# Kernel tuning notes

Measured on AMD Instinct MI355X. Metric: run time of the kernel, lower is better.

## Reference

```python
import jax, jax.numpy as jnp
import numpy as np

B, T, N, F, H, R, E = 32, 8, 150, 16, 32, 4, 16


def _gconv(X, Af, Wf):
    # t-product graph conv (Kilmer t-product = circular conv over relation axis,
    # implemented facewise in the Fourier domain): ifft( fft(adj) @ fft(X) @ fft(W) )
    Xf = jnp.fft.fft(X, axis=-1)                      # [b,n,f,r] complex
    Y = jnp.einsum('nmr,bmfr->bnfr', Af, Xf)          # aggregate over nodes
    Y = jnp.einsum('bnfr,for->bnor', Y, Wf)           # feature transform
    return jnp.fft.ifft(Y, axis=-1).real


def _cell(X, Hs, Af, Wf, Bb):
    # TensorGRUCell. NOTE: faithful to the source, H_tilda reuses conv_hr
    # (conv_hh is defined but never used in the original forward).
    Wxz, Wxr, Wxh, Whz, Whr = Wf
    bz, br, bh = Bb[0], Bb[1], Bb[2]                  # [H,R], broadcasts over [b,n,H,R]
    Z = jax.nn.sigmoid(_gconv(X, Af, Wxz) + _gconv(Hs, Af, Whz) + bz)
    Rg = jax.nn.sigmoid(_gconv(X, Af, Wxr) + _gconv(Hs, Af, Whr) + br)
    Ht = jnp.tanh(_gconv(X, Af, Wxh) + _gconv(Rg * Hs, Af, Whr) + bh)
    return Z * Hs + (1.0 - Z) * Ht


def setup_inputs() -> dict:
    key = jax.random.key(0)
    ks = jax.random.split(key, 16)
    kai = lambda k, shp, fan: (jax.random.normal(k, shp, jnp.float32)
                               * np.float32(np.sqrt(2.0 / fan)))
    d = {}
    d['inputs'] = jax.random.normal(ks[0], (B, T, N, F, R), jnp.float32)
    d['U'] = kai(ks[1], (N, E, R), N)
    # layer 0 (input_dim=F)
    d['Wxz0'] = kai(ks[2], (F, H, R), F)
    d['Wxr0'] = kai(ks[3], (F, H, R), F)
    d['Wxh0'] = kai(ks[4], (F, H, R), F)
    d['Whz0'] = kai(ks[5], (H, H, R), H)
    d['Whr0'] = kai(ks[6], (H, H, R), H)
    d['B0'] = kai(ks[7], (3, H, R), 3)
    # layer 1 (input_dim=H)
    d['Wxz1'] = kai(ks[8], (H, H, R), H)
    d['Wxr1'] = kai(ks[9], (H, H, R), H)
    d['Wxh1'] = kai(ks[10], (H, H, R), H)
    d['Whz1'] = kai(ks[11], (H, H, R), H)
    d['Whr1'] = kai(ks[12], (H, H, R), H)
    d['B1'] = kai(ks[13], (3, H, R), 3)
    return d


def reference(inputs, U, Wxz0, Wxr0, Wxh0, Whz0, Whr0, B0,
              Wxz1, Wxr1, Wxh1, Whz1, Whr1, B1):
    # adaptive adjacency: softmax(relu(tprod(U, U^T)), dim=1)
    Uf = jnp.fft.fft(U, axis=-1)                      # [N,E,R] complex
    A = jnp.fft.ifft(jnp.einsum('ner,mer->nmr', Uf, Uf), axis=-1).real
    adj = jax.nn.softmax(jax.nn.relu(A), axis=1)      # [N,N,R]

    Af = jnp.fft.fft(adj, axis=-1)
    Wf0 = tuple(jnp.fft.fft(w, axis=-1) for w in (Wxz0, Wxr0, Wxh0, Whz0, Whr0))
    Wf1 = tuple(jnp.fft.fft(w, axis=-1) for w in (Wxz1, Wxr1, Wxh1, Whz1, Whr1))

    b, t, n, f, r = inputs.shape
    h = Whz0.shape[0]
    z0 = jnp.zeros((b, n, h, r), inputs.dtype)

    # t = 0: layer1 consumes the *current* layer0 output
    o0 = _cell(inputs[:, 0], z0, Af, Wf0, B0)
    o1 = _cell(o0, z0, Af, Wf1, B1)

    # t > 0: faithful to source, layer1 consumes the *previous timestep's*
    # layer0 output (temp_out[t-1][i-1]) with hidden temp_out[t-1][i].
    def step(carry, Xt):
        p0, p1 = carry
        n0 = _cell(Xt, p0, Af, Wf0, B0)
        n1 = _cell(p0, p1, Af, Wf1, B1)
        return (n0, n1), n1

    Xs = jnp.moveaxis(inputs[:, 1:], 1, 0)            # [T-1,B,N,F,R]
    (c0, c1), ys = jax.lax.scan(step, (o0, o1), Xs)

    out = jnp.concatenate([o1[None], ys], axis=0)     # [T,B,N,H,R]
    out = jnp.moveaxis(out, 0, 1)                     # [B,T,N,H,R]
    h_last = jnp.stack([c0, c1])                      # [L,B,N,H,R]
    return out, h_last
```

## Files before the change

kernel.cpp:

```cpp
#include <hip/hip_runtime.h>
#include <math.h>

#define NN 150
#define BB 32
#define TT 8
#define FF 16
#define HH 32
#define ROWS (NN*BB)
#define NCIN (BB*FF)
#define NCH  (BB*HH)
#define ADJ_LD 160
#define KPAD 68

#define SZ_ADJF (4*NN*ADJ_LD)
#define SZ_WA0  (4*48*32*4)
#define SZ_WA1  (4*64*32*4)
#define SZ_WB   (32*32*4)
#define SZ_STATE (ROWS*HH*4)
#define SZ_PIN  (4*NN*NCIN)

__device__ __forceinline__ float sigmoidf_(float x){ return 1.f/(1.f+expf(-x)); }

__device__ __forceinline__ float comp_of4(float x0, float x1, float x2, float x3, int c) {
  return c==0 ? (x0+x1+x2+x3) : c==1 ? (x0-x2) : c==2 ? (x3-x1) : (x0-x1+x2-x3);
}


__global__ __launch_bounds__(256) void k_adj(const float* __restrict__ U, float* __restrict__ adjF) {
  __shared__ float Ufl[NN*16*4];
  __shared__ float Arow[NN*4];
  __shared__ float red[256];
  __shared__ float mxs[4], isms[4];
  int n = blockIdx.x, tid = threadIdx.x;
  for (int idx = tid; idx < NN*16; idx += 256) {
    const float* s = U + (size_t)idx*4;
    float x0=s[0], x1=s[1], x2=s[2], x3=s[3];
    Ufl[idx*4+0] = x0+x1+x2+x3;
    Ufl[idx*4+1] = x0-x2;
    Ufl[idx*4+2] = x3-x1;
    Ufl[idx*4+3] = x0-x1+x2-x3;
  }
  __syncthreads();
  if (tid < NN) {
    int m = tid;
    float a0=0, ar=0, ai=0, a2=0;
    #pragma unroll
    for (int e = 0; e < 16; ++e) {
      const float* un = &Ufl[(n*16+e)*4];
      const float* um = &Ufl[(m*16+e)*4];
      a0 += un[0]*um[0];
      ar += un[1]*um[1] - un[2]*um[2];
      ai += un[1]*um[2] + un[2]*um[1];
      a2 += un[3]*um[3];
    }
    float r0 = 0.25f*(a0 + 2.f*ar + a2);
    float r1 = 0.25f*(a0 - 2.f*ai - a2);
    float r2 = 0.25f*(a0 - 2.f*ar + a2);
    float r3 = 0.25f*(a0 + 2.f*ai - a2);
    Arow[m*4+0] = fmaxf(r0, 0.f);
    Arow[m*4+1] = fmaxf(r1, 0.f);
    Arow[m*4+2] = fmaxf(r2, 0.f);
    Arow[m*4+3] = fmaxf(r3, 0.f);
  }
  __syncthreads();
  for (int r = 0; r < 4; ++r) {
    float v = (tid < NN) ? Arow[tid*4+r] : -1e30f;
    red[tid] = v; __syncthreads();
    for (int s = 128; s > 0; s >>= 1) { if (tid < s) red[tid] = fmaxf(red[tid], red[tid+s]); __syncthreads(); }
    if (tid == 0) mxs[r] = red[0];
    __syncthreads();
    float e = (tid < NN) ? expf(Arow[tid*4+r] - mxs[r]) : 0.f;
    red[tid] = e; __syncthreads();
    for (int s = 128; s > 0; s >>= 1) { if (tid < s) red[tid] += red[tid+s]; __syncthreads(); }
    if (tid == 0) isms[r] = 1.f / red[0];
    __syncthreads();
    if (tid < NN) Arow[tid*4+r] = e * isms[r];
    __syncthreads();
  }
  if (tid < NN) {
    int m = tid;
    float e0=Arow[m*4+0], e1=Arow[m*4+1], e2=Arow[m*4+2], e3=Arow[m*4+3];
    size_t base = (size_t)n*ADJ_LD + m;
    size_t cs = (size_t)NN*ADJ_LD;
    adjF[base]      = e0+e1+e2+e3;
    adjF[base+cs]   = e0-e2;
    adjF[base+2*cs] = e3-e1;
    adjF[base+3*cs] = e0-e1+e2-e3;
  } else if (tid < ADJ_LD) {
    size_t base = (size_t)n*ADJ_LD + tid;
    size_t cs = (size_t)NN*ADJ_LD;
    adjF[base] = 0.f; adjF[base+cs] = 0.f; adjF[base+2*cs] = 0.f; adjF[base+3*cs] = 0.f;
  }
}

__global__ __launch_bounds__(256) void k_wts(
    const float* __restrict__ Wxz0, const float* __restrict__ Wxr0, const float* __restrict__ Wxh0,
    const float* __restrict__ Whz0, const float* __restrict__ Whr0,
    const float* __restrict__ Wxz1, const float* __restrict__ Wxr1, const float* __restrict__ Wxh1,
    const float* __restrict__ Whz1, const float* __restrict__ Whr1,
    float* __restrict__ WA0p, float* __restrict__ WA1p,
    float* __restrict__ WB0p, float* __restrict__ WB1p) {
  int idx = blockIdx.x*256 + threadIdx.x;
  const float* src = nullptr;
  float* dst; int didx; int c;
  if (idx < SZ_WA0) {
    c = idx / 6144;
    int rem = idx % 6144;
    int k = rem >> 7, og = (rem >> 2) & 31, q = rem & 3;
    if (q == 0) src = (k < FF) ? Wxz0 + ((size_t)k*HH + og)*4 : Whz0 + ((size_t)(k-FF)*HH + og)*4;
    else if (q == 1) src = (k < FF) ? Wxr0 + ((size_t)k*HH + og)*4 : Whr0 + ((size_t)(k-FF)*HH + og)*4;
    else if (q == 2 && k < FF) src = Wxh0 + ((size_t)k*HH + og)*4;
    dst = WA0p; didx = idx;
  } else if (idx < SZ_WA0 + SZ_WA1) {
    int id = idx - SZ_WA0;
    c = id >> 13;
    int rem = id & 8191;
    int k = rem >> 7, og = (rem >> 2) & 31, q = rem & 3;
    if (q == 0) src = (k < HH) ? Wxz1 + ((size_t)k*HH + og)*4 : Whz1 + ((size_t)(k-HH)*HH + og)*4;
    else if (q == 1) src = (k < HH) ? Wxr1 + ((size_t)k*HH + og)*4 : Whr1 + ((size_t)(k-HH)*HH + og)*4;
    else if (q == 2 && k < HH) src = Wxh1 + ((size_t)k*HH + og)*4;
    dst = WA1p; didx = id;
  } else if (idx < SZ_WA0 + SZ_WA1 + SZ_WB) {
    int id = idx - (SZ_WA0 + SZ_WA1);
    int k = id >> 7, o = (id >> 2) & 31;
    c = id & 3;
    src = Whr0 + ((size_t)k*HH + o)*4;
    dst = WB0p; didx = id;
  } else if (idx < SZ_WA0 + SZ_WA1 + 2*SZ_WB) {
    int id = idx - (SZ_WA0 + SZ_WA1 + SZ_WB);
    int k = id >> 7, o = (id >> 2) & 31;
    c = id & 3;
    src = Whr1 + ((size_t)k*HH + o)*4;
    dst = WB1p; didx = id;
  } else return;
  float v0=0,v1=0,v2=0,v3=0;
  if (src) { v0=src[0]; v1=src[1]; v2=src[2]; v3=src[3]; }
  dst[didx] = comp_of4(v0,v1,v2,v3,c);
}

struct AggParams {
  const float* X0; const float* X1; const float* X2;
  float* P0; float* P1; float* P2;
  int ncol0, ncol1, ncol2;
  int base1, base2, njobs, rawt, nb;
};
__global__ __launch_bounds__(256,4) void k_agg(AggParams pr, const float* __restrict__ adjF,
                                               const float* __restrict__ inp) {
  __shared__ float As[4*32*37];
  __shared__ float Xs[4*32*36];
  int bid = blockIdx.x;
  int part = (bid >= pr.nb) ? 1 : 0;
  if (part) bid -= pr.nb;
  const float* X; float* P; int ncol; int tile; bool raw = false;
  if (pr.njobs >= 3 && bid >= pr.base2) { X = pr.X2; P = pr.P2; ncol = pr.ncol2; tile = bid - pr.base2; }
  else if (pr.njobs >= 2 && bid >= pr.base1) { X = pr.X1; P = pr.P1; ncol = pr.ncol1; tile = bid - pr.base1; }
  else { X = pr.X0; P = pr.P0; ncol = pr.ncol0; tile = bid; raw = (pr.rawt >= 0); }
  P += (size_t)part * 4 * NN * ncol;
  int kbeg = part ? 96 : 0;
  int kend = part ? NN : 96;
  int n0 = (tile % 5) * 32;
  int col0 = (tile / 5) * 32;
  int tid = threadIdx.x;
  int ti = tid & 31, tj = tid >> 5;
  int j0 = tj * 4;
  float a0[4]={}, aR[4]={}, aI[4]={}, a2v[4]={};

  float4 pa[4];
  float4 px[4];

  #define LOAD_A(K0)                                                         \
    _Pragma("unroll")                                                        \
    for (int u = 0; u < 4; ++u) {                                            \
      int e = tid + u*256;                                                   \
      int c = e >> 8, rem = e & 255, i = rem >> 3, kq = rem & 7;             \
      int nn_ = n0 + i;                                                      \
      pa[u] = make_float4(0,0,0,0);                                          \
      if (nn_ < NN) pa[u] = *(const float4*)(adjF + ((size_t)c*NN + nn_)*ADJ_LD + (K0) + kq*4); \
    }
  #define STORE_A()                                                          \
    _Pragma("unroll")                                                        \
    for (int u = 0; u < 4; ++u) {                                            \
      int e = tid + u*256;                                                   \
      int c = e >> 8, rem = e & 255, i = rem >> 3, kq = rem & 7;             \
      As[(c*32 + kq*4+0)*37 + i] = pa[u].x;                                  \
      As[(c*32 + kq*4+1)*37 + i] = pa[u].y;                                  \
      As[(c*32 + kq*4+2)*37 + i] = pa[u].z;                                  \
      As[(c*32 + kq*4+3)*37 + i] = pa[u].w;                                  \
    }
  #define LOAD_X(K0)                                                         \
    if (raw) {                                                               \
      int q = tid & 7, kk = tid >> 3;                                        \
      int mm = (K0) + kk;                                                    \
      int col = col0 + q*4;                                                  \
      int b = col >> 4, f = col & 15;                                        \
      px[0]=px[1]=px[2]=px[3]=make_float4(0,0,0,0);                          \
      if (mm < NN) {                                                         \
        const float* s = inp + (((size_t)(b*TT + pr.rawt)*NN + mm)*FF + f)*4;\
        px[0] = *(const float4*)(s+0);                                       \
        px[1] = *(const float4*)(s+4);                                       \
        px[2] = *(const float4*)(s+8);                                       \
        px[3] = *(const float4*)(s+12);                                      \
      }                                                                      \
    } else {                                                                 \
      _Pragma("unroll")                                                      \
      for (int u = 0; u < 4; ++u) {                                          \
        int e = tid + u*256;                                                 \
        int c = e >> 8, rem = e & 255, kk = rem >> 3, q = rem & 7;           \
        int mm = (K0) + kk;                                                  \
        px[u] = make_float4(0,0,0,0);                                        \
        if (mm < NN) px[u] = *(const float4*)(X + ((size_t)c*NN + mm)*ncol + col0 + q*4); \
      }                                                                      \
    }
  #define STORE_X()                                                          \
    if (raw) {                                                               \
      int q = tid & 7, kk = tid >> 3;                                        \
      float4 r0 = px[0], r1 = px[1], r2 = px[2], r3 = px[3];                 \
      float4 w;                                                              \
      w = make_float4(r0.x+r0.y+r0.z+r0.w, r1.x+r1.y+r1.z+r1.w, r2.x+r2.y+r2.z+r2.w, r3.x+r3.y+r3.z+r3.w); \
      *(float4*)&Xs[(0*32+kk)*36 + q*4] = w;                                 \
      w = make_float4(r0.x-r0.z, r1.x-r1.z, r2.x-r2.z, r3.x-r3.z);           \
      *(float4*)&Xs[(1*32+kk)*36 + q*4] = w;                                 \
      w = make_float4(r0.w-r0.y, r1.w-r1.y, r2.w-r2.y, r3.w-r3.y);           \
      *(float4*)&Xs[(2*32+kk)*36 + q*4] = w;                                 \
      w = make_float4(r0.x-r0.y+r0.z-r0.w, r1.x-r1.y+r1.z-r1.w, r2.x-r2.y+r2.z-r2.w, r3.x-r3.y+r3.z-r3.w); \
      *(float4*)&Xs[(3*32+kk)*36 + q*4] = w;                                 \
    } else {                                                                 \
      _Pragma("unroll")                                                      \
      for (int u = 0; u < 4; ++u) {                                          \
        int e = tid + u*256;                                                 \
        int c = e >> 8, rem = e & 255, kk = rem >> 3, q = rem & 7;           \
        *(float4*)&Xs[(c*32+kk)*36 + q*4] = px[u];                           \
      }                                                                      \
    }

  LOAD_A(kbeg)
  LOAD_X(kbeg)
  for (int k0 = kbeg; k0 < kend; k0 += 32) {
    STORE_A()
    STORE_X()
    __syncthreads();
    int k0n = k0 + 32;
    if (k0n < kend) {
      LOAD_A(k0n)
      LOAD_X(k0n)
    }
    #pragma unroll 4
    for (int k = 0; k < 32; ++k) {
      float A0 = As[(0*32+k)*37 + ti];
      float A1 = As[(1*32+k)*37 + ti];
      float A2 = As[(2*32+k)*37 + ti];
      float A3 = As[(3*32+k)*37 + ti];
      float4 x0 = *(float4*)&Xs[(0*32+k)*36 + j0];
      float4 x1 = *(float4*)&Xs[(1*32+k)*36 + j0];
      float4 x2 = *(float4*)&Xs[(2*32+k)*36 + j0];
      float4 x3 = *(float4*)&Xs[(3*32+k)*36 + j0];
      float X0v[4]={x0.x,x0.y,x0.z,x0.w}, X1v[4]={x1.x,x1.y,x1.z,x1.w};
      float X2v[4]={x2.x,x2.y,x2.z,x2.w}, X3v[4]={x3.x,x3.y,x3.z,x3.w};
      #pragma unroll
      for (int j = 0; j < 4; ++j) {
        a0[j] += A0*X0v[j];
        aR[j] += A1*X1v[j] - A2*X2v[j];
        aI[j] += A1*X2v[j] + A2*X1v[j];
        a2v[j] += A3*X3v[j];
      }
    }
    __syncthreads();
  }
  int nn_ = n0 + ti;
  if (nn_ < NN) {
    size_t cs = (size_t)NN*ncol;
    size_t rb = (size_t)nn_*ncol + col0 + j0;
    *(float4*)&P[rb]      = make_float4(a0[0],a0[1],a0[2],a0[3]);
    *(float4*)&P[rb+cs]   = make_float4(aR[0],aR[1],aR[2],aR[3]);
    *(float4*)&P[rb+2*cs] = make_float4(aI[0],aI[1],aI[2],aI[3]);
    *(float4*)&P[rb+3*cs] = make_float4(a2v[0],a2v[1],a2v[2],a2v[3]);
  }
}

struct FAJob {
  const float* Px;
  const float* Ph;
  const float* W;
  const float* bias;
  const float* hprev;
  float* Z; float* T1; float* Mf;
  int zh;
};
struct FAParams { FAJob j[2]; };

template<int KTOT, int KX>
__device__ __forceinline__ void fusedA_body(const FAJob& jb, float* Ps, float* Ws) {
  const int row0 = blockIdx.x * 16;
  const int tid = threadIdx.x;
  const int og = tid & 31;
  const int rg = tid >> 5;
  const int r0 = rg*2, r1 = rg*2 + 1;
  const size_t psx = (size_t)4*ROWS*KX;
  const size_t psh = (size_t)4*ROWS*HH;
  constexpr int K4 = KTOT/4;
  for (int e = tid; e < 16*4*K4; e += 256) {
    int k4 = e % K4; int c = (e / K4) & 3; int r = e / (K4*4);
    int k = k4*4;
    int row = row0 + r;
    float4 v;
    if (k < KX) {
      const float* a = &jb.Px[((size_t)c*ROWS + row)*KX + k];
      float4 va = *(const float4*)a;
      float4 vb = *(const float4*)(a + psx);
      v = make_float4(va.x+vb.x, va.y+vb.y, va.z+vb.z, va.w+vb.w);
    } else if (jb.zh) {
      v = make_float4(0,0,0,0);
    } else {
      const float* a = &jb.Ph[((size_t)c*ROWS + row)*HH + (k - KX)];
      float4 va = *(const float4*)a;
      float4 vb = *(const float4*)(a + psh);
      v = make_float4(va.x+vb.x, va.y+vb.y, va.z+vb.z, va.w+vb.w);
    }
    *(float4*)&Ps[(r*4 + c)*KPAD + k] = v;
  }
  float acc0[2][3]={{0,0,0},{0,0,0}}, accR[2][3]={{0,0,0},{0,0,0}};
  float accI[2][3]={{0,0,0},{0,0,0}}, acc2[2][3]={{0,0,0},{0,0,0}};
  constexpr int NCHK = KTOT/16;
  const float4* Wg = (const float4*)jb.W;
  for (int cc = 0; cc < NCHK; ++cc) {
    __syncthreads();
    #pragma unroll
    for (int u = 0; u < 8; ++u) {
      int f = tid + u*256;
      int c = f >> 9, rem = f & 511;
      float4 v = Wg[((size_t)c*KTOT + cc*16)*32 + rem];
      *(float4*)&Ws[((size_t)c*512 + rem)*4] = v;
    }
    __syncthreads();
    #pragma unroll 4
    for (int kk = 0; kk < 16; ++kk) {
      int k = cc*16 + kk;
      float p0a = Ps[(r0*4+0)*KPAD + k];
      float p1a = Ps[(r0*4+1)*KPAD + k];
      float p2a = Ps[(r0*4+2)*KPAD + k];
      float p3a = Ps[(r0*4+3)*KPAD + k];
      float p0b = Ps[(r1*4+0)*KPAD + k];
      float p1b = Ps[(r1*4+1)*KPAD + k];
      float p2b = Ps[(r1*4+2)*KPAD + k];
      float p3b = Ps[(r1*4+3)*KPAD + k];
      float4 w0 = *(float4*)&Ws[((0*16+kk)*32+og)*4];
      float4 w1 = *(float4*)&Ws[((1*16+kk)*32+og)*4];
      float4 w2 = *(float4*)&Ws[((2*16+kk)*32+og)*4];
      float4 w3 = *(float4*)&Ws[((3*16+kk)*32+og)*4];
      float W0v[3]={w0.x,w0.y,w0.z}, W1v[3]={w1.x,w1.y,w1.z};
      float W2v[3]={w2.x,w2.y,w2.z}, W3v[3]={w3.x,w3.y,w3.z};
      #pragma unroll
      for (int q = 0; q < 3; ++q) {
        acc0[0][q] += p0a*W0v[q];
        acc0[1][q] += p0b*W0v[q];
        accR[0][q] += p1a*W1v[q] - p2a*W2v[q];
        accR[1][q] += p1b*W1v[q] - p2b*W2v[q];
        accI[0][q] += p1a*W2v[q] + p2a*W1v[q];
        accI[1][q] += p1b*W2v[q] + p2b*W1v[q];
        acc2[0][q] += p3a*W3v[q];
        acc2[1][q] += p3b*W3v[q];
      }
    }
  }
  const float* bz = jb.bias + (0*HH + og)*4;
  const float* br = jb.bias + (1*HH + og)*4;
  const float* bh = jb.bias + (2*HH + og)*4;
  float bzv[4] = {bz[0],bz[1],bz[2],bz[3]};
  float brv[4] = {br[0],br[1],br[2],br[3]};
  float bhv[4] = {bh[0],bh[1],bh[2],bh[3]};
  #pragma unroll
  for (int rr = 0; rr < 2; ++rr) {
    int row = row0 + rg*2 + rr;
    float ys[3][4];
    #pragma unroll
    for (int q = 0; q < 3; ++q) {
      float Y0 = acc0[rr][q], Yr = accR[rr][q], Yi = accI[rr][q], Y2 = acc2[rr][q];
      ys[q][0] = 0.25f*(Y0 + 2.f*Yr + Y2);
      ys[q][1] = 0.25f*(Y0 - 2.f*Yi - Y2);
      ys[q][2] = 0.25f*(Y0 - 2.f*Yr + Y2);
      ys[q][3] = 0.25f*(Y0 + 2.f*Yi - Y2);
    }
    float4 z = make_float4(sigmoidf_(ys[0][0]+bzv[0]), sigmoidf_(ys[0][1]+bzv[1]),
                           sigmoidf_(ys[0][2]+bzv[2]), sigmoidf_(ys[0][3]+bzv[3]));
    *(float4*)&jb.Z[((size_t)row*HH + og)*4] = z;
    float4 hp = make_float4(0,0,0,0);
    if (!jb.zh) hp = *(const float4*)&jb.hprev[((size_t)row*HH + og)*4];
    float m0 = sigmoidf_(ys[1][0]+brv[0]) * hp.x;
    float m1 = sigmoidf_(ys[1][1]+brv[1]) * hp.y;
    float m2 = sigmoidf_(ys[1][2]+brv[2]) * hp.z;
    float m3 = sigmoidf_(ys[1][3]+brv[3]) * hp.w;
    size_t mb = (size_t)row*HH + og;
    size_t cs = (size_t)ROWS*HH;
    jb.Mf[mb]      = m0+m1+m2+m3;
    jb.Mf[mb+cs]   = m0-m2;
    jb.Mf[mb+2*cs] = m3-m1;
    jb.Mf[mb+3*cs] = m0-m1+m2-m3;
    float4 tv = make_float4(ys[2][0]+bhv[0], ys[2][1]+bhv[1], ys[2][2]+bhv[2], ys[2][3]+bhv[3]);
    *(float4*)&jb.T1[((size_t)row*HH + og)*4] = tv;
  }
}

__global__ __launch_bounds__(256,3) void k_fusedA_both(FAParams pr) {
  __shared__ float Ps[16*4*KPAD];
  __shared__ float Ws[8192];
  if (blockIdx.y == 0) fusedA_body<48,16>(pr.j[0], Ps, Ws);
  else                 fusedA_body<64,32>(pr.j[1], Ps, Ws);
}
__global__ __launch_bounds__(256,3) void k_fusedA_L0(FAParams pr) {
  __shared__ float Ps[16*4*KPAD];
  __shared__ float Ws[8192];
  fusedA_body<48,16>(pr.j[0], Ps, Ws);
}
__global__ __launch_bounds__(256,3) void k_fusedA_L1(FAParams pr) {
  __shared__ float Ps[16*4*KPAD];
  __shared__ float Ws[8192];
  fusedA_body<64,32>(pr.j[1], Ps, Ws);
}

struct FBJob {
  const float* Pm; const float* W; const float* T1; const float* Z;
  float* h; float* hf; float* outp; float* hlast;
  int t, zh, wout;
};
struct FBParams { FBJob j[2]; };
__global__ __launch_bounds__(256,4) void k_fusedB(FBParams pr) {
  __shared__ float Ps[16*32*4];
  __shared__ float Ws[32*32*4];
  FBJob jb = pr.j[blockIdx.y];
  int row0 = blockIdx.x * 16;
  int tid = threadIdx.x;
  int rg = tid >> 5, o = tid & 31;
  int r0 = rg*2, r1 = r0 + 1;
  float acc0[2]={0,0}, accR[2]={0,0}, accI[2]={0,0}, acc2[2]={0,0};
  if (!jb.zh) {
    #pragma unroll
    for (int u = 0; u < 4; ++u) {
      int f = tid + u*256;
      ((float4*)Ws)[f] = ((const float4*)jb.W)[f];
    }
    const size_t psh = (size_t)4*ROWS*HH;
    #pragma unroll
    for (int u = 0; u < 2; ++u) {
      int e = tid + u*256;
      int r = e >> 5, k = e & 31;
      int row = row0 + r;
      float4 v;
      float* vv = (float*)&v;
      #pragma unroll
      for (int c = 0; c < 4; ++c) {
        size_t ix = ((size_t)c*ROWS + row)*HH + k;
        vv[c] = jb.Pm[ix] + jb.Pm[ix + psh];
      }
      *(float4*)&Ps[(r*32 + k)*4] = v;
    }
    __syncthreads();
    #pragma unroll 8
    for (int k = 0; k < 32; ++k) {
      float4 pA = *(const float4*)&Ps[(r0*32 + k)*4];
      float4 pB = *(const float4*)&Ps[(r1*32 + k)*4];
      float4 w  = *(const float4*)&Ws[(k*32 + o)*4];
      acc0[0] += pA.x*w.x;  acc0[1] += pB.x*w.x;
      accR[0] += pA.y*w.y - pA.z*w.z;  accR[1] += pB.y*w.y - pB.z*w.z;
      accI[0] += pA.y*w.z + pA.z*w.y;  accI[1] += pB.y*w.z + pB.z*w.y;
      acc2[0] += pA.w*w.w;  acc2[1] += pB.w*w.w;
    }
  }
  #pragma unroll
  for (int rr = 0; rr < 2; ++rr) {
    int row = row0 + rg*2 + rr;
    float y0 = 0.25f*(acc0[rr] + 2.f*accR[rr] + acc2[rr]);
    float y1 = 0.25f*(acc0[rr] - 2.f*accI[rr] - acc2[rr]);
    float y2 = 0.25f*(acc0[rr] - 2.f*accR[rr] + acc2[rr]);
    float y3 = 0.25f*(acc0[rr] + 2.f*accI[rr] - acc2[rr]);
    float4 t1 = *(const float4*)&jb.T1[((size_t)row*HH + o)*4];
    float h0v = tanhf(t1.x + y0);
    float h1v = tanhf(t1.y + y1);
    float h2v = tanhf(t1.z + y2);
    float h3v = tanhf(t1.w + y3);
    float4 z = *(const float4*)&jb.Z[((size_t)row*HH + o)*4];
    float4 hp = make_float4(0,0,0,0);
    if (!jb.zh) hp = *(const float4*)&jb.h[((size_t)row*HH + o)*4];
    float n0v = z.x*hp.x + (1.f-z.x)*h0v;
    float n1v = z.y*hp.y + (1.f-z.y)*h1v;
    float n2v = z.z*hp.z + (1.f-z.z)*h2v;
    float n3v = z.w*hp.w + (1.f-z.w)*h3v;
    *(float4*)&jb.h[((size_t)row*HH + o)*4] = make_float4(n0v,n1v,n2v,n3v);
    size_t hb = (size_t)row*HH + o, cs = (size_t)ROWS*HH;
    jb.hf[hb]      = n0v+n1v+n2v+n3v;
    jb.hf[hb+cs]   = n0v-n2v;
    jb.hf[hb+2*cs] = n3v-n1v;
    jb.hf[hb+3*cs] = n0v-n1v+n2v-n3v;
    int n = row >> 5, b = row & 31;
    if (jb.wout) {
      float* dst = jb.outp + (((size_t)b*TT + jb.t)*NN + n)*(HH*4) + o*4;
      *(float4*)dst = make_float4(n0v,n1v,n2v,n3v);
    }
    if (jb.hlast) {
      float* dst = jb.hlast + ((size_t)(b*NN + n))*(HH*4) + o*4;
      *(float4*)dst = make_float4(n0v,n1v,n2v,n3v);
    }
  }
}

extern "C" void kernel_launch(void* const* d_in, const int* in_sizes, int n_in,
                              void* d_out, int out_size, void* d_ws, size_t ws_size,
                              hipStream_t stream) {
  const float* inp  = (const float*)d_in[0];
  const float* U    = (const float*)d_in[1];
  const float* Wxz0 = (const float*)d_in[2];
  const float* Wxr0 = (const float*)d_in[3];
  const float* Wxh0 = (const float*)d_in[4];
  const float* Whz0 = (const float*)d_in[5];
  const float* Whr0 = (const float*)d_in[6];
  const float* B0   = (const float*)d_in[7];
  const float* Wxz1 = (const float*)d_in[8];
  const float* Wxr1 = (const float*)d_in[9];
  const float* Wxh1 = (const float*)d_in[10];
  const float* Whz1 = (const float*)d_in[11];
  const float* Whr1 = (const float*)d_in[12];
  const float* B1   = (const float*)d_in[13];
  float* out = (float*)d_out;

  float* ws = (float*)d_ws;
  float* ADJF = ws;  ws += SZ_ADJF;
  float* WA0  = ws;  ws += SZ_WA0;
  float* WA1  = ws;  ws += SZ_WA1;
  float* WB0  = ws;  ws += SZ_WB;
  float* WB1  = ws;  ws += SZ_WB;
  float* H0   = ws;  ws += SZ_STATE;
  float* H1   = ws;  ws += SZ_STATE;
  float* H0F  = ws;  ws += SZ_STATE;
  float* H1F  = ws;  ws += SZ_STATE;
  float* PIN  = ws;  ws += 2*SZ_PIN;
  float* PH0  = ws;  ws += 2*SZ_STATE;
  float* PH1  = ws;  ws += 2*SZ_STATE;
  float* PM0  = ws;  ws += 2*SZ_STATE;
  float* PM1  = ws;  ws += 2*SZ_STATE;
  float* M0F  = ws;  ws += SZ_STATE;
  float* M1F  = ws;  ws += SZ_STATE;
  float* Z0   = ws;  ws += SZ_STATE;
  float* Z1   = ws;  ws += SZ_STATE;
  float* T10  = ws;  ws += SZ_STATE;
  float* T11  = ws;  ws += SZ_STATE;

  k_adj<<<NN, 256, 0, stream>>>(U, ADJF);
  k_wts<<<(SZ_WA0+SZ_WA1+2*SZ_WB+255)/256, 256, 0, stream>>>(
      Wxz0,Wxr0,Wxh0,Whz0,Whr0,Wxz1,Wxr1,Wxh1,Whz1,Whr1,WA0,WA1,WB0,WB1);

  {
    AggParams p; p.X0=nullptr; p.P0=PIN; p.ncol0=NCIN;
    p.X1=nullptr; p.P1=nullptr; p.ncol1=0; p.X2=nullptr; p.P2=nullptr; p.ncol2=0;
    p.base1=0; p.base2=0; p.njobs=1; p.rawt=0; p.nb=80;
    k_agg<<<160, 256, 0, stream>>>(p, ADJF, inp);
  }
  {
    FAParams p;
    p.j[0] = FAJob{PIN, nullptr, WA0, B0, nullptr, Z0, T10, M0F, 1};
    p.j[1] = p.j[0];
    k_fusedA_L0<<<dim3(300,1), 256, 0, stream>>>(p);
  }
  {
    FBParams p;
    p.j[0] = FBJob{nullptr, WB0, T10, Z0, H0, H0F, nullptr, nullptr, 0, 1, 0};
    p.j[1] = p.j[0];
    k_fusedB<<<dim3(300,1), 256, 0, stream>>>(p);
  }
  {
    AggParams p; p.X0=H0F; p.P0=PH0; p.ncol0=NCH;
    p.X1=nullptr; p.P1=nullptr; p.ncol1=0; p.X2=nullptr; p.P2=nullptr; p.ncol2=0;
    p.base1=0; p.base2=0; p.njobs=1; p.rawt=-1; p.nb=160;
    k_agg<<<320, 256, 0, stream>>>(p, ADJF, inp);
  }
  {
    FAParams p;
    p.j[0] = FAJob{PH0, nullptr, WA1, B1, nullptr, Z1, T11, M1F, 1};
    p.j[1] = p.j[0];
    k_fusedA_L1<<<dim3(300,1), 256, 0, stream>>>(p);
  }
  {
    FBParams p;
    p.j[0] = FBJob{nullptr, WB1, T11, Z1, H1, H1F, out, nullptr, 0, 1, 1};
    p.j[1] = p.j[0];
    k_fusedB<<<dim3(300,1), 256, 0, stream>>>(p);
  }

  float* hlast0 = out + (size_t)BB*TT*NN*HH*4;
  float* hlast1 = hlast0 + (size_t)BB*NN*HH*4;
  for (int t = 1; t < TT; ++t) {
    {
      AggParams p;
      p.X0=nullptr; p.P0=PIN; p.ncol0=NCIN;
      p.X1=H0F; p.P1=PH0; p.ncol1=NCH;
      p.X2=H1F; p.P2=PH1; p.ncol2=NCH;
      p.base1=80; p.base2=240; p.njobs=3; p.rawt=t; p.nb=400;
      k_agg<<<800, 256, 0, stream>>>(p, ADJF, inp);
    }
    {
      FAParams p;
      p.j[0] = FAJob{PIN, PH0, WA0, B0, H0, Z0, T10, M0F, 0};
      p.j[1] = FAJob{PH0, PH1, WA1, B1, H1, Z1, T11, M1F, 0};
      k_fusedA_both<<<dim3(300,2), 256, 0, stream>>>(p);
    }
    {
      AggParams p;
      p.X0=M0F; p.P0=PM0; p.ncol0=NCH;
      p.X1=M1F; p.P1=PM1; p.ncol1=NCH;
      p.X2=nullptr; p.P2=nullptr; p.ncol2=0;
      p.base1=160; p.base2=0; p.njobs=2; p.rawt=-1; p.nb=320;
      k_agg<<<640, 256, 0, stream>>>(p, ADJF, inp);
    }
    {
      int last = (t == TT-1);
      FBParams p;
      p.j[0] = FBJob{PM0, WB0, T10, Z0, H0, H0F, nullptr, last ? hlast0 : nullptr, t, 0, 0};
      p.j[1] = FBJob{PM1, WB1, T11, Z1, H1, H1F, out,     last ? hlast1 : nullptr, t, 0, 1};
      k_fusedB<<<dim3(300,2), 256, 0, stream>>>(p);
    }
  }
}
```

Baseline: 846.2 us.

## Hoist input aggregation for all timesteps out of recurrence and interleave shared-memory layouts

Precomputes the adjacency aggregation of the raw inputs for every timestep in one up-front launch, removing that work from each recurrent step's aggregation kernel. Merges the adjacency and weight-prep kernels into one launch. Also changes the shared-memory layouts of the aggregation A tile and the fusedA P tile so the four Fourier components are interleaved, allowing single float4 reads. The cost is a larger workspace holding all timesteps' aggregated inputs.

```diff
diff --git a/kernel.cpp b/kernel.cpp
--- a/kernel.cpp
+++ b/kernel.cpp
@@ -10,7 +10,7 @@
 #define NCIN (BB*FF)
 #define NCH  (BB*HH)
 #define ADJ_LD 160
-#define KPAD 68
+#define PS_LD 65
 
 #define SZ_ADJF (4*NN*ADJ_LD)
 #define SZ_WA0  (4*48*32*4)
@@ -26,81 +26,83 @@
 }
 
 
-__global__ __launch_bounds__(256) void k_adj(const float* __restrict__ U, float* __restrict__ adjF) {
-  __shared__ float Ufl[NN*16*4];
-  __shared__ float Arow[NN*4];
-  __shared__ float red[256];
-  __shared__ float mxs[4], isms[4];
-  int n = blockIdx.x, tid = threadIdx.x;
-  for (int idx = tid; idx < NN*16; idx += 256) {
-    const float* s = U + (size_t)idx*4;
-    float x0=s[0], x1=s[1], x2=s[2], x3=s[3];
-    Ufl[idx*4+0] = x0+x1+x2+x3;
-    Ufl[idx*4+1] = x0-x2;
-    Ufl[idx*4+2] = x3-x1;
-    Ufl[idx*4+3] = x0-x1+x2-x3;
-  }
-  __syncthreads();
-  if (tid < NN) {
-    int m = tid;
-    float a0=0, ar=0, ai=0, a2=0;
-    #pragma unroll
-    for (int e = 0; e < 16; ++e) {
-      const float* un = &Ufl[(n*16+e)*4];
-      const float* um = &Ufl[(m*16+e)*4];
-      a0 += un[0]*um[0];
-      ar += un[1]*um[1] - un[2]*um[2];
-      ai += un[1]*um[2] + un[2]*um[1];
-      a2 += un[3]*um[3];
-    }
-    float r0 = 0.25f*(a0 + 2.f*ar + a2);
-    float r1 = 0.25f*(a0 - 2.f*ai - a2);
-    float r2 = 0.25f*(a0 - 2.f*ar + a2);
-    float r3 = 0.25f*(a0 + 2.f*ai - a2);
-    Arow[m*4+0] = fmaxf(r0, 0.f);
-    Arow[m*4+1] = fmaxf(r1, 0.f);
-    Arow[m*4+2] = fmaxf(r2, 0.f);
-    Arow[m*4+3] = fmaxf(r3, 0.f);
-  }
-  __syncthreads();
-  for (int r = 0; r < 4; ++r) {
-    float v = (tid < NN) ? Arow[tid*4+r] : -1e30f;
-    red[tid] = v; __syncthreads();
-    for (int s = 128; s > 0; s >>= 1) { if (tid < s) red[tid] = fmaxf(red[tid], red[tid+s]); __syncthreads(); }
-    if (tid == 0) mxs[r] = red[0];
-    __syncthreads();
-    float e = (tid < NN) ? expf(Arow[tid*4+r] - mxs[r]) : 0.f;
-    red[tid] = e; __syncthreads();
-    for (int s = 128; s > 0; s >>= 1) { if (tid < s) red[tid] += red[tid+s]; __syncthreads(); }
-    if (tid == 0) isms[r] = 1.f / red[0];
-    __syncthreads();
-    if (tid < NN) Arow[tid*4+r] = e * isms[r];
-    __syncthreads();
-  }
-  if (tid < NN) {
-    int m = tid;
-    float e0=Arow[m*4+0], e1=Arow[m*4+1], e2=Arow[m*4+2], e3=Arow[m*4+3];
-    size_t base = (size_t)n*ADJ_LD + m;
-    size_t cs = (size_t)NN*ADJ_LD;
-    adjF[base]      = e0+e1+e2+e3;
-    adjF[base+cs]   = e0-e2;
-    adjF[base+2*cs] = e3-e1;
-    adjF[base+3*cs] = e0-e1+e2-e3;
-  } else if (tid < ADJ_LD) {
-    size_t base = (size_t)n*ADJ_LD + tid;
-    size_t cs = (size_t)NN*ADJ_LD;
-    adjF[base] = 0.f; adjF[base+cs] = 0.f; adjF[base+2*cs] = 0.f; adjF[base+3*cs] = 0.f;
-  }
-}
-
-__global__ __launch_bounds__(256) void k_wts(
+__global__ __launch_bounds__(256) void k_pre(
+    const float* __restrict__ U, float* __restrict__ adjF,
     const float* __restrict__ Wxz0, const float* __restrict__ Wxr0, const float* __restrict__ Wxh0,
     const float* __restrict__ Whz0, const float* __restrict__ Whr0,
     const float* __restrict__ Wxz1, const float* __restrict__ Wxr1, const float* __restrict__ Wxh1,
     const float* __restrict__ Whz1, const float* __restrict__ Whr1,
     float* __restrict__ WA0p, float* __restrict__ WA1p,
     float* __restrict__ WB0p, float* __restrict__ WB1p) {
-  int idx = blockIdx.x*256 + threadIdx.x;
+  __shared__ float Ufl[NN*16*4];
+  __shared__ float Arow[NN*4];
+  __shared__ float red[256];
+  __shared__ float mxs[4], isms[4];
+  int tid = threadIdx.x;
+  if (blockIdx.x < NN) {
+    int n = blockIdx.x;
+    for (int idx = tid; idx < NN*16; idx += 256) {
+      const float* s = U + (size_t)idx*4;
+      float x0=s[0], x1=s[1], x2=s[2], x3=s[3];
+      Ufl[idx*4+0] = x0+x1+x2+x3;
+      Ufl[idx*4+1] = x0-x2;
+      Ufl[idx*4+2] = x3-x1;
+      Ufl[idx*4+3] = x0-x1+x2-x3;
+    }
+    __syncthreads();
+    if (tid < NN) {
+      int m = tid;
+      float a0=0, ar=0, ai=0, a2=0;
+      #pragma unroll
+      for (int e = 0; e < 16; ++e) {
+        const float* un = &Ufl[(n*16+e)*4];
+        const float* um = &Ufl[(m*16+e)*4];
+        a0 += un[0]*um[0];
+        ar += un[1]*um[1] - un[2]*um[2];
+        ai += un[1]*um[2] + un[2]*um[1];
+        a2 += un[3]*um[3];
+      }
+      float r0 = 0.25f*(a0 + 2.f*ar + a2);
+      float r1 = 0.25f*(a0 - 2.f*ai - a2);
+      float r2 = 0.25f*(a0 - 2.f*ar + a2);
+      float r3 = 0.25f*(a0 + 2.f*ai - a2);
+      Arow[m*4+0] = fmaxf(r0, 0.f);
+      Arow[m*4+1] = fmaxf(r1, 0.f);
+      Arow[m*4+2] = fmaxf(r2, 0.f);
+      Arow[m*4+3] = fmaxf(r3, 0.f);
+    }
+    __syncthreads();
+    for (int r = 0; r < 4; ++r) {
+      float v = (tid < NN) ? Arow[tid*4+r] : -1e30f;
+      red[tid] = v; __syncthreads();
+      for (int s = 128; s > 0; s >>= 1) { if (tid < s) red[tid] = fmaxf(red[tid], red[tid+s]); __syncthreads(); }
+      if (tid == 0) mxs[r] = red[0];
+      __syncthreads();
+      float e = (tid < NN) ? expf(Arow[tid*4+r] - mxs[r]) : 0.f;
+      red[tid] = e; __syncthreads();
+      for (int s = 128; s > 0; s >>= 1) { if (tid < s) red[tid] += red[tid+s]; __syncthreads(); }
+      if (tid == 0) isms[r] = 1.f / red[0];
+      __syncthreads();
+      if (tid < NN) Arow[tid*4+r] = e * isms[r];
+      __syncthreads();
+    }
+    if (tid < NN) {
+      int m = tid;
+      float e0=Arow[m*4+0], e1=Arow[m*4+1], e2=Arow[m*4+2], e3=Arow[m*4+3];
+      size_t base = (size_t)n*ADJ_LD + m;
+      size_t cs = (size_t)NN*ADJ_LD;
+      adjF[base]      = e0+e1+e2+e3;
+      adjF[base+cs]   = e0-e2;
+      adjF[base+2*cs] = e3-e1;
+      adjF[base+3*cs] = e0-e1+e2-e3;
+    } else if (tid < ADJ_LD) {
+      size_t base = (size_t)n*ADJ_LD + tid;
+      size_t cs = (size_t)NN*ADJ_LD;
+      adjF[base] = 0.f; adjF[base+cs] = 0.f; adjF[base+2*cs] = 0.f; adjF[base+3*cs] = 0.f;
+    }
+    return;
+  }
+  int idx = (blockIdx.x - NN)*256 + tid;
   const float* src = nullptr;
   float* dst; int didx; int c;
   if (idx < SZ_WA0) {
@@ -138,35 +140,21 @@
   dst[didx] = comp_of4(v0,v1,v2,v3,c);
 }
 
-struct AggParams {
-  const float* X0; const float* X1; const float* X2;
-  float* P0; float* P1; float* P2;
-  int ncol0, ncol1, ncol2;
-  int base1, base2, njobs, rawt, nb;
-};
-__global__ __launch_bounds__(256,4) void k_agg(AggParams pr, const float* __restrict__ adjF,
-                                               const float* __restrict__ inp) {
-  __shared__ float As[4*32*37];
-  __shared__ float Xs[4*32*36];
-  int bid = blockIdx.x;
-  int part = (bid >= pr.nb) ? 1 : 0;
-  if (part) bid -= pr.nb;
-  const float* X; float* P; int ncol; int tile; bool raw = false;
-  if (pr.njobs >= 3 && bid >= pr.base2) { X = pr.X2; P = pr.P2; ncol = pr.ncol2; tile = bid - pr.base2; }
-  else if (pr.njobs >= 2 && bid >= pr.base1) { X = pr.X1; P = pr.P1; ncol = pr.ncol1; tile = bid - pr.base1; }
-  else { X = pr.X0; P = pr.P0; ncol = pr.ncol0; tile = bid; raw = (pr.rawt >= 0); }
-  P += (size_t)part * 4 * NN * ncol;
+template<bool RAW>
+__device__ __forceinline__ void agg_body(const float* __restrict__ adjF,
+                                         const float* __restrict__ X,
+                                         const float* __restrict__ inp,
+                                         float* __restrict__ P, int ncol,
+                                         int tile, int part, int rawt,
+                                         float* As, float* Xs, int tid) {
   int kbeg = part ? 96 : 0;
   int kend = part ? NN : 96;
   int n0 = (tile % 5) * 32;
   int col0 = (tile / 5) * 32;
-  int tid = threadIdx.x;
   int ti = tid & 31, tj = tid >> 5;
   int j0 = tj * 4;
   float a0[4]={}, aR[4]={}, aI[4]={}, a2v[4]={};
-
-  float4 pa[4];
-  float4 px[4];
+  float4 pa[4], px[4];
 
   #define LOAD_A(K0)                                                         \
     _Pragma("unroll")                                                        \
@@ -182,20 +170,20 @@
     for (int u = 0; u < 4; ++u) {                                            \
       int e = tid + u*256;                                                   \
       int c = e >> 8, rem = e & 255, i = rem >> 3, kq = rem & 7;             \
-      As[(c*32 + kq*4+0)*37 + i] = pa[u].x;                                  \
-      As[(c*32 + kq*4+1)*37 + i] = pa[u].y;                                  \
-      As[(c*32 + kq*4+2)*37 + i] = pa[u].z;                                  \
-      As[(c*32 + kq*4+3)*37 + i] = pa[u].w;                                  \
+      As[((kq*4+0)*33 + i)*4 + c] = pa[u].x;                                 \
+      As[((kq*4+1)*33 + i)*4 + c] = pa[u].y;                                 \
+      As[((kq*4+2)*33 + i)*4 + c] = pa[u].z;                                 \
+      As[((kq*4+3)*33 + i)*4 + c] = pa[u].w;                                 \
     }
   #define LOAD_X(K0)                                                         \
-    if (raw) {                                                               \
+    if (RAW) {                                                               \
       int q = tid & 7, kk = tid >> 3;                                        \
       int mm = (K0) + kk;                                                    \
       int col = col0 + q*4;                                                  \
       int b = col >> 4, f = col & 15;                                        \
       px[0]=px[1]=px[2]=px[3]=make_float4(0,0,0,0);                          \
       if (mm < NN) {                                                         \
-        const float* s = inp + (((size_t)(b*TT + pr.rawt)*NN + mm)*FF + f)*4;\
+        const float* s = inp + (((size_t)(b*TT + rawt)*NN + mm)*FF + f)*4;   \
         px[0] = *(const float4*)(s+0);                                       \
         px[1] = *(const float4*)(s+4);                                       \
         px[2] = *(const float4*)(s+8);                                       \
@@ -212,7 +200,7 @@
       }                                                                      \
     }
   #define STORE_X()                                                          \
-    if (raw) {                                                               \
+    if (RAW) {                                                               \
       int q = tid & 7, kk = tid >> 3;                                        \
       float4 r0 = px[0], r1 = px[1], r2 = px[2], r3 = px[3];                 \
       float4 w;                                                              \
@@ -246,10 +234,7 @@
     }
     #pragma unroll 4
     for (int k = 0; k < 32; ++k) {
-      float A0 = As[(0*32+k)*37 + ti];
-      float A1 = As[(1*32+k)*37 + ti];
-      float A2 = As[(2*32+k)*37 + ti];
-      float A3 = As[(3*32+k)*37 + ti];
+      float4 a4 = *(float4*)&As[(k*33 + ti)*4];
       float4 x0 = *(float4*)&Xs[(0*32+k)*36 + j0];
       float4 x1 = *(float4*)&Xs[(1*32+k)*36 + j0];
       float4 x2 = *(float4*)&Xs[(2*32+k)*36 + j0];
@@ -258,14 +243,18 @@
       float X2v[4]={x2.x,x2.y,x2.z,x2.w}, X3v[4]={x3.x,x3.y,x3.z,x3.w};
       #pragma unroll
       for (int j = 0; j < 4; ++j) {
-        a0[j] += A0*X0v[j];
-        aR[j] += A1*X1v[j] - A2*X2v[j];
-        aI[j] += A1*X2v[j] + A2*X1v[j];
-        a2v[j] += A3*X3v[j];
+        a0[j]  += a4.x*X0v[j];
+        aR[j]  += a4.y*X1v[j] - a4.z*X2v[j];
+        aI[j]  += a4.y*X2v[j] + a4.z*X1v[j];
+        a2v[j] += a4.w*X3v[j];
       }
     }
     __syncthreads();
   }
+  #undef LOAD_A
+  #undef STORE_A
+  #undef LOAD_X
+  #undef STORE_X
   int nn_ = n0 + ti;
   if (nn_ < NN) {
     size_t cs = (size_t)NN*ncol;
@@ -275,6 +264,38 @@
     *(float4*)&P[rb+2*cs] = make_float4(aI[0],aI[1],aI[2],aI[3]);
     *(float4*)&P[rb+3*cs] = make_float4(a2v[0],a2v[1],a2v[2],a2v[3]);
   }
+}
+
+#define AGG_AS 4224
+#define AGG_XS 4608
+
+__global__ __launch_bounds__(256,4) void k_aggIN(const float* __restrict__ adjF,
+                                                 const float* __restrict__ inp,
+                                                 float* __restrict__ PIN) {
+  __shared__ float As[AGG_AS];
+  __shared__ float Xs[AGG_XS];
+  int u = blockIdx.x;
+  int t = u / 160, rem = u % 160, part = rem / 80, tile = rem % 80;
+  float* P = PIN + (size_t)t*2*SZ_PIN + (size_t)part*SZ_PIN;
+  agg_body<true>(adjF, nullptr, inp, P, NCIN, tile, part, t, As, Xs, threadIdx.x);
+}
+
+struct AggParams {
+  const float* X0; const float* X1;
+  float* P0; float* P1;
+  int base1, njobs, nb;
+};
+__global__ __launch_bounds__(256,4) void k_agg(AggParams pr, const float* __restrict__ adjF) {
+  __shared__ float As[AGG_AS];
+  __shared__ float Xs[AGG_XS];
+  int bid = blockIdx.x;
+  int part = (bid >= pr.nb) ? 1 : 0;
+  if (part) bid -= pr.nb;
+  const float* X; float* P; int tile;
+  if (pr.njobs >= 2 && bid >= pr.base1) { X = pr.X1; P = pr.P1; tile = bid - pr.base1; }
+  else { X = pr.X0; P = pr.P0; tile = bid; }
+  P += (size_t)part * SZ_STATE;
+  agg_body<false>(adjF, X, nullptr, P, NCH, tile, part, -1, As, Xs, threadIdx.x);
 }
 
 struct FAJob {
@@ -316,7 +337,10 @@
       float4 vb = *(const float4*)(a + psh);
       v = make_float4(va.x+vb.x, va.y+vb.y, va.z+vb.z, va.w+vb.w);
     }
-    *(float4*)&Ps[(r*4 + c)*KPAD + k] = v;
+    Ps[(r*PS_LD + k+0)*4 + c] = v.x;
+    Ps[(r*PS_LD + k+1)*4 + c] = v.y;
+    Ps[(r*PS_LD + k+2)*4 + c] = v.z;
+    Ps[(r*PS_LD + k+3)*4 + c] = v.w;
   }
   float acc0[2][3]={{0,0,0},{0,0,0}}, accR[2][3]={{0,0,0},{0,0,0}};
   float accI[2][3]={{0,0,0},{0,0,0}}, acc2[2][3]={{0,0,0},{0,0,0}};
@@ -335,14 +359,8 @@
     #pragma unroll 4
     for (int kk = 0; kk < 16; ++kk) {
       int k = cc*16 + kk;
-      float p0a = Ps[(r0*4+0)*KPAD + k];
-      float p1a = Ps[(r0*4+1)*KPAD + k];
-      float p2a = Ps[(r0*4+2)*KPAD + k];
-      float p3a = Ps[(r0*4+3)*KPAD + k];
-      float p0b = Ps[(r1*4+0)*KPAD + k];
-      float p1b = Ps[(r1*4+1)*KPAD + k];
-      float p2b = Ps[(r1*4+2)*KPAD + k];
-      float p3b = Ps[(r1*4+3)*KPAD + k];
+      float4 pA = *(float4*)&Ps[(r0*PS_LD + k)*4];
+      float4 pB = *(float4*)&Ps[(r1*PS_LD + k)*4];
       float4 w0 = *(float4*)&Ws[((0*16+kk)*32+og)*4];
       float4 w1 = *(float4*)&Ws[((1*16+kk)*32+og)*4];
       float4 w2 = *(float4*)&Ws[((2*16+kk)*32+og)*4];
@@ -351,14 +369,14 @@
       float W2v[3]={w2.x,w2.y,w2.z}, W3v[3]={w3.x,w3.y,w3.z};
       #pragma unroll
       for (int q = 0; q < 3; ++q) {
-        acc0[0][q] += p0a*W0v[q];
-        acc0[1][q] += p0b*W0v[q];
-        accR[0][q] += p1a*W1v[q] - p2a*W2v[q];
-        accR[1][q] += p1b*W1v[q] - p2b*W2v[q];
-        accI[0][q] += p1a*W2v[q] + p2a*W1v[q];
-        accI[1][q] += p1b*W2v[q] + p2b*W1v[q];
-        acc2[0][q] += p3a*W3v[q];
-        acc2[1][q] += p3b*W3v[q];
+        acc0[0][q] += pA.x*W0v[q];
+        acc0[1][q] += pB.x*W0v[q];
+        accR[0][q] += pA.y*W1v[q] - pA.z*W2v[q];
+        accR[1][q] += pB.y*W1v[q] - pB.z*W2v[q];
+        accI[0][q] += pA.y*W2v[q] + pA.z*W1v[q];
+        accI[1][q] += pB.y*W2v[q] + pB.z*W1v[q];
+        acc2[0][q] += pA.w*W3v[q];
+        acc2[1][q] += pB.w*W3v[q];
       }
     }
   }
@@ -400,19 +418,21 @@
   }
 }
 
+#define FA_PS (16*PS_LD*4)
+
 __global__ __launch_bounds__(256,3) void k_fusedA_both(FAParams pr) {
-  __shared__ float Ps[16*4*KPAD];
+  __shared__ float Ps[FA_PS];
   __shared__ float Ws[8192];
   if (blockIdx.y == 0) fusedA_body<48,16>(pr.j[0], Ps, Ws);
   else                 fusedA_body<64,32>(pr.j[1], Ps, Ws);
 }
 __global__ __launch_bounds__(256,3) void k_fusedA_L0(FAParams pr) {
-  __shared__ float Ps[16*4*KPAD];
+  __shared__ float Ps[FA_PS];
   __shared__ float Ws[8192];
   fusedA_body<48,16>(pr.j[0], Ps, Ws);
 }
 __global__ __launch_bounds__(256,3) void k_fusedA_L1(FAParams pr) {
-  __shared__ float Ps[16*4*KPAD];
+  __shared__ float Ps[FA_PS];
   __shared__ float Ws[8192];
   fusedA_body<64,32>(pr.j[1], Ps, Ws);
 }
@@ -531,7 +551,7 @@
   float* H1   = ws;  ws += SZ_STATE;
   float* H0F  = ws;  ws += SZ_STATE;
   float* H1F  = ws;  ws += SZ_STATE;
-  float* PIN  = ws;  ws += 2*SZ_PIN;
+  float* PIN  = ws;  ws += (size_t)TT*2*SZ_PIN;
   float* PH0  = ws;  ws += 2*SZ_STATE;
   float* PH1  = ws;  ws += 2*SZ_STATE;
   float* PM0  = ws;  ws += 2*SZ_STATE;
@@ -543,16 +563,14 @@
   float* T10  = ws;  ws += SZ_STATE;
   float* T11  = ws;  ws += SZ_STATE;
 
-  k_adj<<<NN, 256, 0, stream>>>(U, ADJF);
-  k_wts<<<(SZ_WA0+SZ_WA1+2*SZ_WB+255)/256, 256, 0, stream>>>(
-      Wxz0,Wxr0,Wxh0,Whz0,Whr0,Wxz1,Wxr1,Wxh1,Whz1,Whr1,WA0,WA1,WB0,WB1);
-
-  {
-    AggParams p; p.X0=nullptr; p.P0=PIN; p.ncol0=NCIN;
-    p.X1=nullptr; p.P1=nullptr; p.ncol1=0; p.X2=nullptr; p.P2=nullptr; p.ncol2=0;
-    p.base1=0; p.base2=0; p.njobs=1; p.rawt=0; p.nb=80;
-    k_agg<<<160, 256, 0, stream>>>(p, ADJF, inp);
-  }
+  k_pre<<<NN + (SZ_WA0+SZ_WA1+2*SZ_WB+255)/256, 256, 0, stream>>>(
+      U, ADJF, Wxz0,Wxr0,Wxh0,Whz0,Whr0, Wxz1,Wxr1,Wxh1,Whz1,Whr1, WA0,WA1,WB0,WB1);
+
+  k_aggIN<<<TT*2*80, 256, 0, stream>>>(ADJF, inp, PIN);
+
+  float* hlast0 = out + (size_t)BB*TT*NN*HH*4;
+  float* hlast1 = hlast0 + (size_t)BB*NN*HH*4;
+
   {
     FAParams p;
     p.j[0] = FAJob{PIN, nullptr, WA0, B0, nullptr, Z0, T10, M0F, 1};
@@ -566,10 +584,9 @@
     k_fusedB<<<dim3(300,1), 256, 0, stream>>>(p);
   }
   {
-    AggParams p; p.X0=H0F; p.P0=PH0; p.ncol0=NCH;
-    p.X1=nullptr; p.P1=nullptr; p.ncol1=0; p.X2=nullptr; p.P2=nullptr; p.ncol2=0;
-    p.base1=0; p.base2=0; p.njobs=1; p.rawt=-1; p.nb=160;
-    k_agg<<<320, 256, 0, stream>>>(p, ADJF, inp);
+    AggParams p; p.X0=H0F; p.P0=PH0; p.X1=nullptr; p.P1=nullptr;
+    p.base1=0; p.njobs=1; p.nb=160;
+    k_agg<<<320, 256, 0, stream>>>(p, ADJF);
   }
   {
     FAParams p;
@@ -584,30 +601,22 @@
     k_fusedB<<<dim3(300,1), 256, 0, stream>>>(p);
   }
 
-  float* hlast0 = out + (size_t)BB*TT*NN*HH*4;
-  float* hlast1 = hlast0 + (size_t)BB*NN*HH*4;
   for (int t = 1; t < TT; ++t) {
     {
-      AggParams p;
-      p.X0=nullptr; p.P0=PIN; p.ncol0=NCIN;
-      p.X1=H0F; p.P1=PH0; p.ncol1=NCH;
-      p.X2=H1F; p.P2=PH1; p.ncol2=NCH;
-      p.base1=80; p.base2=240; p.njobs=3; p.rawt=t; p.nb=400;
-      k_agg<<<800, 256, 0, stream>>>(p, ADJF, inp);
+      AggParams p; p.X0=H0F; p.P0=PH0; p.X1=H1F; p.P1=PH1;
+      p.base1=160; p.njobs=2; p.nb=320;
+      k_agg<<<640, 256, 0, stream>>>(p, ADJF);
     }
     {
       FAParams p;
-      p.j[0] = FAJob{PIN, PH0, WA0, B0, H0, Z0, T10, M0F, 0};
+      p.j[0] = FAJob{PIN + (size_t)t*2*SZ_PIN, PH0, WA0, B0, H0, Z0, T10, M0F, 0};
       p.j[1] = FAJob{PH0, PH1, WA1, B1, H1, Z1, T11, M1F, 0};
       k_fusedA_both<<<dim3(300,2), 256, 0, stream>>>(p);
     }
     {
-      AggParams p;
-      p.X0=M0F; p.P0=PM0; p.ncol0=NCH;
-      p.X1=M1F; p.P1=PM1; p.ncol1=NCH;
-      p.X2=nullptr; p.P2=nullptr; p.ncol2=0;
-      p.base1=160; p.base2=0; p.njobs=2; p.rawt=-1; p.nb=320;
-      k_agg<<<640, 256, 0, stream>>>(p, ADJF, inp);
+      AggParams p; p.X0=M0F; p.P0=PM0; p.X1=M1F; p.P1=PM1;
+      p.base1=160; p.njobs=2; p.nb=320;
+      k_agg<<<640, 256, 0, stream>>>(p, ADJF);
     }
     {
       int last = (t == TT-1);
```

Result: no change. 830.2 us (-1.9%).
